# Performance work log

Measured on AMD Instinct MI355X. Metric: run time of the kernel, lower is better.

Reference implementation:

```python
import jax, jax.numpy as jnp
import numpy as np

# Dimensions (all layers are mLSTM due to the constructor bug: `if w` tests the
# whole truthy `which` list, so signature=(2,1) still yields 3 mLSTM layers).
L, S, B, I = 3, 512, 4, 512      # layers, seq_len, batch, inp_dim
H, D = 8, 64                     # head_num, head_dim
HD = H * D                       # hidden dim = 512
P = 2 * I                        # up_l projection dim (m-branch p_factor = 2)
K = 4                            # causal conv kernel size
EPS = 1e-5
PNAMES = ['ln_g', 'ln_b', 'upl_w', 'upl_b', 'upr_w', 'upr_b', 'conv_w', 'conv_b',
          'wq_w', 'wq_b', 'wk_w', 'wk_b', 'wv_w', 'wv_b', 'wo_w', 'wo_b',
          'wi_w', 'wi_b', 'wf_w', 'wf_b', 'skip_w', 'gn_g', 'gn_b', 'down_w', 'down_b']


def setup_inputs() -> dict:
    key = jax.random.key(0)
    ks = iter(jax.random.split(key, 16))
    def w(shape, fan_in):
        return jax.random.normal(next(ks), shape, jnp.float32) / np.float32(np.sqrt(fan_in))
    return {
        'seq': jax.random.normal(next(ks), (S, B, I), jnp.float32),
        'ln_g': jnp.ones((L, I), jnp.float32), 'ln_b': jnp.zeros((L, I), jnp.float32),
        'upl_w': w((L, P, I), I), 'upl_b': jnp.zeros((L, P), jnp.float32),
        'upr_w': w((L, HD, I), I), 'upr_b': jnp.zeros((L, HD), jnp.float32),
        'conv_w': w((L, K), K), 'conv_b': jnp.zeros((L,), jnp.float32),
        'wq_w': w((L, HD, P), P), 'wq_b': jnp.zeros((L, HD), jnp.float32),
        'wk_w': w((L, HD, P), P), 'wk_b': jnp.zeros((L, HD), jnp.float32),
        'wv_w': w((L, HD, P), P), 'wv_b': jnp.zeros((L, HD), jnp.float32),
        'wo_w': w((L, HD, P), P), 'wo_b': jnp.zeros((L, HD), jnp.float32),
        'wi_w': w((L, H, P), P), 'wi_b': jnp.zeros((L, H), jnp.float32),
        'wf_w': w((L, H, P), P), 'wf_b': jnp.zeros((L, H), jnp.float32),
        'skip_w': w((L, HD, P), P),
        'gn_g': jnp.ones((L, HD), jnp.float32), 'gn_b': jnp.zeros((L, HD), jnp.float32),
        'down_w': w((L, I, HD), HD), 'down_b': jnp.zeros((L, I), jnp.float32),
    }


def _layernorm(x, g, b):
    mu = x.mean(-1, keepdims=True)
    v = ((x - mu) ** 2).mean(-1, keepdims=True)
    return (x - mu) / jnp.sqrt(v + EPS) * g + b


def _groupnorm(x, g, b):
    # GroupNorm(head_num, HD) on (B, HD): normalize each head's D channels
    xh = x.reshape(-1, H, D)
    mu = xh.mean(-1, keepdims=True)
    v = ((xh - mu) ** 2).mean(-1, keepdims=True)
    xn = (xh - mu) / jnp.sqrt(v + EPS)
    return (xn * g.reshape(H, D) + b.reshape(H, D)).reshape(-1, HD)


def _causal_conv(x, w, b):
    # 1-channel causal conv over the feature axis of the per-step vector (B, P)
    xp = jnp.pad(x, ((0, 0), (K - 1, 0)))
    y = b
    for k in range(K):  # K=4, static unroll
        y = y + w[k] * xp[:, k:k + x.shape[1]]
    return y


def _mlstm_step(p, x, state):
    c_, n_, m_ = state
    x_n = _layernorm(x, p['ln_g'], p['ln_b'])
    x_t = x_n @ p['upl_w'].T + p['upl_b']                 # (B, P)
    r_t = x_n @ p['upr_w'].T + p['upr_b']                 # (B, HD)
    x_c = jax.nn.silu(_causal_conv(x_t, p['conv_w'], p['conv_b']))
    q = (x_c @ p['wq_w'].T + p['wq_b']).reshape(-1, H, D)
    k = (x_c @ p['wk_w'].T + p['wk_b']).reshape(-1, H, D) / np.float32(np.sqrt(D))
    v = (x_t @ p['wv_w'].T + p['wv_b']).reshape(-1, H, D)
    i = x_c @ p['wi_w'].T + p['wi_b']                     # (B, H)
    f = x_c @ p['wf_w'].T + p['wf_b']                     # (B, H)
    o = jax.nn.sigmoid(x_t @ p['wo_w'].T + p['wo_b'])     # (B, HD)
    m = jnp.maximum(f + m_, i)                            # stabilizer
    ig = jnp.exp(i - m)
    fg = jnp.exp(f - m + m_)
    c = fg[..., None, None] * c_ + ig[..., None, None] * jnp.einsum('bhd,bhe->bhde', v, k)
    n = fg[..., None] * n_ + ig[..., None] * k
    num = jnp.einsum('bhde,bhe->bhd', c, q)
    den = jnp.maximum(jnp.abs(jnp.einsum('bhd,bhd->bh', n, q)), 1.0)[..., None]
    h = o * (num / den).reshape(-1, HD)
    out = _groupnorm(h, p['gn_g'], p['gn_b']) + x_c @ p['skip_w'].T
    out = out * jax.nn.silu(r_t)
    out = out @ p['down_w'].T + p['down_b']
    return out + x, (c, n, m)


def _forward(seq, params):
    b = seq.shape[1]
    def step(states, x_t):
        new_states = []
        inp = x_t
        for l in range(L):
            pl = {k: v[l] for k, v in params.items()}
            inp, st = _mlstm_step(pl, inp, states[l])
            new_states.append(st)
        return tuple(new_states), inp
    init = tuple((jnp.zeros((b, H, D, D), seq.dtype),
                  jnp.ones((b, H, D), seq.dtype),
                  jnp.zeros((b, H), seq.dtype)) for _ in range(L))
    _, out = jax.lax.scan(step, init, seq)
    return out  # (S, B, I)


def reference(seq, ln_g, ln_b, upl_w, upl_b, upr_w, upr_b, conv_w, conv_b,
              wq_w, wq_b, wk_w, wk_b, wv_w, wv_b, wo_w, wo_b,
              wi_w, wi_b, wf_w, wf_b, skip_w, gn_g, gn_b, down_w, down_b):
    params = dict(zip(PNAMES, [ln_g, ln_b, upl_w, upl_b, upr_w, upr_b, conv_w, conv_b,
                               wq_w, wq_b, wk_w, wk_b, wv_w, wv_b, wo_w, wo_b,
                               wi_w, wi_b, wf_w, wf_b, skip_w, gn_g, gn_b, down_w, down_b]))
    return _forward(seq, params)
```

## Files before the change

### kernel.cpp

```cpp
#include <hip/hip_runtime.h>
#include <hip/hip_bf16.h>
#include <cstdint>
#include <cstddef>

typedef short short8 __attribute__((ext_vector_type(8)));
typedef short short4v __attribute__((ext_vector_type(4)));
typedef float f32x4 __attribute__((ext_vector_type(4)));
typedef __hip_bfloat16 bf16;

#define NROW 2048
#define N1 1536
#define N2 1664
#define N3 1024
#define EPSV 1e-5f

static __device__ __forceinline__ bf16 f2bf(float v){ return __float2bfloat16(v); }
static __device__ __forceinline__ float bfbits2f(short s){
  unsigned u = ((unsigned)(unsigned short)s) << 16;
  float f; __builtin_memcpy(&f, &u, 4); return f;
}
static __device__ __forceinline__ void split_bf(float v, bf16& h, bf16& l){
  h = __float2bfloat16(v);
  l = __float2bfloat16(v - __bfloat162float(h));
}

static __device__ __forceinline__ void gload16(const bf16* g, bf16* l){
  __builtin_amdgcn_global_load_lds(
      (const __attribute__((address_space(1))) void*)(g),
      (__attribute__((address_space(3))) void*)(l), 16, 0, 0);
}

#define MFMA __builtin_amdgcn_mfma_f32_16x16x32_bf16

__global__ __launch_bounds__(256) void pack_all(
    const float* __restrict__ upl, const float* __restrict__ upr,
    const float* __restrict__ wq,  const float* __restrict__ wk,
    const float* __restrict__ skp, const float* __restrict__ wi,
    const float* __restrict__ wf,  const float* __restrict__ wv,
    const float* __restrict__ wo,  const float* __restrict__ dw,
    const float* __restrict__ uplb, const float* __restrict__ uprb,
    const float* __restrict__ wqb,  const float* __restrict__ wkb,
    const float* __restrict__ wib,  const float* __restrict__ wfb,
    const float* __restrict__ wvb,  const float* __restrict__ wob,
    const float* __restrict__ dwb,
    bf16* __restrict__ W1h, bf16* __restrict__ W1l,
    bf16* __restrict__ W2h, bf16* __restrict__ W2l,
    bf16* __restrict__ W3h, bf16* __restrict__ W3l,
    bf16* __restrict__ W4h, bf16* __restrict__ W4l,
    float* __restrict__ b1, float* __restrict__ b2,
    float* __restrict__ b3, float* __restrict__ b4)
{
  int l = blockIdx.y;
  int bx = blockIdx.x;
  if (bx < 1536){
    int r = bx;
    const float* src = (r < 1024) ? upl + ((size_t)l*1024 + r)*512
                                  : upr + ((size_t)l*512 + (r-1024))*512;
    size_t o = ((size_t)l*N1 + r)*512;
    for (int c = threadIdx.x; c < 512; c += 256) split_bf(src[c], W1h[o+c], W1l[o+c]);
  } else if (bx < 3200){
    int r = bx - 1536;
    const float* src; float sc = 1.f;
    if (r < 512)        src = wq  + ((size_t)l*512 + r)*1024;
    else if (r < 1024){ src = wk  + ((size_t)l*512 + r-512)*1024; sc = 0.125f; }
    else if (r < 1536)  src = skp + ((size_t)l*512 + r-1024)*1024;
    else if (r < 1544)  src = wi  + ((size_t)l*8   + r-1536)*1024;
    else if (r < 1552)  src = wf  + ((size_t)l*8   + r-1544)*1024;
    else src = nullptr;
    size_t o = ((size_t)l*N2 + r)*1024;
    for (int c = threadIdx.x; c < 1024; c += 256)
      split_bf(src ? src[c]*sc : 0.f, W2h[o+c], W2l[o+c]);
  } else if (bx < 4224){
    int r = bx - 3200;
    const float* src = (r < 512) ? wv + ((size_t)l*512 + r)*1024
                                 : wo + ((size_t)l*512 + (r-512))*1024;
    size_t o = ((size_t)l*N3 + r)*1024;
    for (int c = threadIdx.x; c < 1024; c += 256) split_bf(src[c], W3h[o+c], W3l[o+c]);
  } else if (bx < 4736){
    int r = bx - 4224;
    const float* src = dw + ((size_t)l*512 + r)*512;
    size_t o = ((size_t)l*512 + r)*512;
    for (int c = threadIdx.x; c < 512; c += 256) split_bf(src[c], W4h[o+c], W4l[o+c]);
  } else {
    for (int j = threadIdx.x; j < N1; j += 256)
      b1[l*N1+j] = (j < 1024) ? uplb[l*1024+j] : uprb[l*512+j-1024];
    for (int j = threadIdx.x; j < N2; j += 256){
      float v = 0.f;
      if (j < 512)        v = wqb[l*512+j];
      else if (j < 1024)  v = wkb[l*512+j-512]*0.125f;
      else if (j < 1536)  v = 0.f;
      else if (j < 1544)  v = wib[l*8+j-1536];
      else if (j < 1552)  v = wfb[l*8+j-1544];
      b2[l*N2+j] = v;
    }
    for (int j = threadIdx.x; j < N3; j += 256)
      b3[l*N3+j] = (j < 512) ? wvb[l*512+j] : wob[l*512+j-512];
    for (int j = threadIdx.x; j < 512; j += 256)
      b4[l*512+j] = dwb[l*512+j];
  }
}

static __device__ __forceinline__ void gemm_core(
    bf16* __restrict__ sm,
    int bx, int by,
    const bf16* __restrict__ Ah, const bf16* __restrict__ Al,
    const bf16* __restrict__ Wh, const bf16* __restrict__ Wl,
    const float* __restrict__ bias, float* __restrict__ Cf,
    bf16* __restrict__ Cbh, bf16* __restrict__ Cbl,
    const float* __restrict__ resid, int N, int K)
{
  int tid = threadIdx.x;
  int lane = tid & 63, w = tid >> 6;
  int wr = w >> 2, wc = w & 3;
  int m0 = by*128, n0 = bx*128;
  int srow = tid >> 2, sslot = tid & 3;
  int gcol = ((sslot ^ (srow & 3)) * 8);
  const bf16* gAh = Ah + (size_t)(m0 + srow)*K + gcol;
  const bf16* gAl = Al + (size_t)(m0 + srow)*K + gcol;
  const bf16* gBh = Wh + (size_t)(n0 + srow)*K + gcol;
  const bf16* gBl = Wl + (size_t)(n0 + srow)*K + gcol;

  f32x4 acc[4][2];
  for (int i=0;i<4;i++) for (int j=0;j<2;j++) acc[i][j] = (f32x4){0.f,0.f,0.f,0.f};

  int r = lane & 15, g = lane >> 4;
  int xs = (g ^ (r & 3)) * 8;
  int aoff[4], boff[2];
  for (int mi=0;mi<4;mi++) aoff[mi] = (wr*64 + mi*16 + r)*32 + xs;
  for (int ni=0;ni<2;ni++) boff[ni] = (wc*32 + ni*16 + r)*32 + xs;

  int nt = K >> 5;
#define STAGE_T(base, kk) do{ bf16* _d = sm + (base) + tid*8; \
    gload16(gAh + (kk), _d); \
    gload16(gAl + (kk), _d + 4096); \
    gload16(gBh + (kk), _d + 8192); \
    gload16(gBl + (kk), _d + 12288); }while(0)

  STAGE_T(0, 0);
  asm volatile("s_waitcnt vmcnt(0)" ::: "memory");
  __builtin_amdgcn_s_barrier();

  for (int t = 0; t < nt; ++t){
    int cb = (t & 1) * 16384;
    if (t + 1 < nt) STAGE_T(16384 - cb, (t+1)*32);
    const bf16* sA = sm + cb;
    short8 ah[4], al[4], bh2[2], bl2[2];
    for (int mi=0;mi<4;mi++){
      ah[mi] = *(const short8*)(sA + aoff[mi]);
      al[mi] = *(const short8*)(sA + 4096 + aoff[mi]);
    }
    for (int ni=0;ni<2;ni++){
      bh2[ni] = *(const short8*)(sA + 8192 + boff[ni]);
      bl2[ni] = *(const short8*)(sA + 12288 + boff[ni]);
    }
    for (int mi=0;mi<4;mi++) for (int ni=0;ni<2;ni++)
      acc[mi][ni] = MFMA(ah[mi], bh2[ni], acc[mi][ni],0,0,0);
    for (int mi=0;mi<4;mi++) for (int ni=0;ni<2;ni++)
      acc[mi][ni] = MFMA(al[mi], bh2[ni], acc[mi][ni],0,0,0);
    for (int mi=0;mi<4;mi++) for (int ni=0;ni<2;ni++)
      acc[mi][ni] = MFMA(ah[mi], bl2[ni], acc[mi][ni],0,0,0);
    asm volatile("s_waitcnt vmcnt(0)" ::: "memory");
    __builtin_amdgcn_s_barrier();
  }
#undef STAGE_T

  for (int mi=0;mi<4;mi++) for (int ni=0;ni<2;ni++){
    int col = n0 + wc*32 + ni*16 + r;
    float bv = bias ? bias[col] : 0.f;
    for (int j=0;j<4;j++){
      int row = m0 + wr*64 + mi*16 + g*4 + j;
      float v = acc[mi][ni][j] + bv;
      size_t o = (size_t)row*N + col;
      if (resid) v += resid[o];
      if (Cf) Cf[o] = v;
      if (Cbh) split_bf(v, Cbh[o], Cbl[o]);
    }
  }
}

static __device__ __forceinline__ void gemm_core64(
    bf16* __restrict__ sm,
    int bx, int by,
    const bf16* __restrict__ Ah, const bf16* __restrict__ Al,
    const bf16* __restrict__ Wh, const bf16* __restrict__ Wl,
    const float* __restrict__ bias, float* __restrict__ Cf,
    bf16* __restrict__ Cbh, bf16* __restrict__ Cbl,
    const float* __restrict__ resid, int N, int K)
{
  int tid = threadIdx.x;
  int lane = tid & 63, w = tid >> 6;
  int m0 = by*64, n0 = bx*128;
  int srow = tid >> 2, sslot = tid & 3;
  int gcol = ((sslot ^ (srow & 3)) * 8);
  const bf16* gAh = Ah + (size_t)(m0 + srow)*K + gcol;
  const bf16* gAl = Al + (size_t)(m0 + srow)*K + gcol;
  const bf16* gBh = Wh + (size_t)(n0 + srow)*K + gcol;
  const bf16* gBl = Wl + (size_t)(n0 + srow)*K + gcol;
  size_t pstr = (size_t)64*K;

  f32x4 acc[4][2];
  for (int i=0;i<4;i++) for (int j=0;j<2;j++) acc[i][j] = (f32x4){0.f,0.f,0.f,0.f};

  int r = lane & 15, g = lane >> 4;
  int xs = (g ^ (r & 3)) * 8;
  int aoff[4], boff[2];
  for (int mi=0;mi<4;mi++) aoff[mi] = (mi*16 + r)*32 + xs;
  for (int ni=0;ni<2;ni++) boff[ni] = (w*32 + ni*16 + r)*32 + xs;

  int nt = K >> 5;
#define STAGE64(base, kk) do{ bf16* _d = sm + (base) + tid*8; \
    gload16(gAh + (kk), _d); \
    gload16(gAl + (kk), _d + 2048); \
    gload16(gBh + (kk), _d + 4096);  gload16(gBh + (kk) + pstr, _d + 6144); \
    gload16(gBl + (kk), _d + 8192);  gload16(gBl + (kk) + pstr, _d + 10240); }while(0)

  STAGE64(0, 0);
  asm volatile("s_waitcnt vmcnt(0)" ::: "memory");
  __builtin_amdgcn_s_barrier();

  for (int t = 0; t < nt; ++t){
    int cb = (t & 1) * 12288;
    if (t + 1 < nt) STAGE64(12288 - cb, (t+1)*32);
    const bf16* sA = sm + cb;
    short8 ah[4], al[4], bh2[2], bl2[2];
    for (int mi=0;mi<4;mi++){
      ah[mi] = *(const short8*)(sA + aoff[mi]);
      al[mi] = *(const short8*)(sA + 2048 + aoff[mi]);
    }
    for (int ni=0;ni<2;ni++){
      bh2[ni] = *(const short8*)(sA + 4096 + boff[ni]);
      bl2[ni] = *(const short8*)(sA + 8192 + boff[ni]);
    }
    for (int mi=0;mi<4;mi++) for (int ni=0;ni<2;ni++)
      acc[mi][ni] = MFMA(ah[mi], bh2[ni], acc[mi][ni],0,0,0);
    for (int mi=0;mi<4;mi++) for (int ni=0;ni<2;ni++)
      acc[mi][ni] = MFMA(al[mi], bh2[ni], acc[mi][ni],0,0,0);
    for (int mi=0;mi<4;mi++) for (int ni=0;ni<2;ni++)
      acc[mi][ni] = MFMA(ah[mi], bl2[ni], acc[mi][ni],0,0,0);
    asm volatile("s_waitcnt vmcnt(0)" ::: "memory");
    __builtin_amdgcn_s_barrier();
  }
#undef STAGE64

  for (int mi=0;mi<4;mi++) for (int ni=0;ni<2;ni++){
    int col = n0 + w*32 + ni*16 + r;
    float bv = bias ? bias[col] : 0.f;
    for (int j=0;j<4;j++){
      int row = m0 + mi*16 + g*4 + j;
      float v = acc[mi][ni][j] + bv;
      size_t o = (size_t)row*N + col;
      if (resid) v += resid[o];
      if (Cf) Cf[o] = v;
      if (Cbh) split_bf(v, Cbh[o], Cbl[o]);
    }
  }
}

__global__ __launch_bounds__(512) void gemm_std(
    const bf16* __restrict__ Ah, const bf16* __restrict__ Al,
    const bf16* __restrict__ Wh, const bf16* __restrict__ Wl,
    const float* __restrict__ bias, float* __restrict__ Cf,
    bf16* __restrict__ Cbh, bf16* __restrict__ Cbl,
    const float* __restrict__ resid, int N, int K, int nbx)
{
  __shared__ bf16 sm[2*4*4096];
  int id = blockIdx.x;
  int cpx = gridDim.x >> 3;
  int swz = (id & 7)*cpx + (id >> 3);
  int by = swz / nbx, bx = swz - by*nbx;
  gemm_core(sm, bx, by, Ah, Al, Wh, Wl, bias, Cf, Cbh, Cbl, resid, N, K);
}

__global__ __launch_bounds__(256) void gemm_s64(
    const bf16* __restrict__ Ah, const bf16* __restrict__ Al,
    const bf16* __restrict__ Wh, const bf16* __restrict__ Wl,
    const float* __restrict__ bias, float* __restrict__ Cf,
    bf16* __restrict__ Cbh, bf16* __restrict__ Cbl,
    const float* __restrict__ resid, int N, int K, int nbx)
{
  __shared__ bf16 sm[2*12288];
  int id = blockIdx.x;
  int cpx = gridDim.x >> 3;
  int swz = (id & 7)*cpx + (id >> 3);
  int by = swz / nbx, bx = swz - by*nbx;
  gemm_core64(sm, bx, by, Ah, Al, Wh, Wl, bias, Cf, Cbh, Cbl, resid, N, K);
}

__global__ __launch_bounds__(512) void gemm23(
    const bf16* __restrict__ A2h, const bf16* __restrict__ A2l,
    const bf16* __restrict__ W2h, const bf16* __restrict__ W2l,
    const float* __restrict__ b2,
    bf16* __restrict__ c2h, bf16* __restrict__ c2l,
    const bf16* __restrict__ A3h, const bf16* __restrict__ A3l,
    const bf16* __restrict__ W3h, const bf16* __restrict__ W3l,
    const float* __restrict__ b3,
    bf16* __restrict__ c3h, bf16* __restrict__ c3l)
{
  __shared__ bf16 sm[2*4*4096];
  int id = blockIdx.x;
  int cpx = gridDim.x >> 3;
  int swz = (id & 7)*cpx + (id >> 3);
  int by = swz / 21, bx = swz - by*21;
  if (bx < 13)
    gemm_core(sm, bx, by, A2h, A2l, W2h, W2l, b2, nullptr, c2h, c2l, nullptr, N2, 1024);
  else
    gemm_core(sm, bx-13, by, A3h, A3l, W3h, W3l, b3, nullptr, c3h, c3l, nullptr, N3, 1024);
}

__global__ __launch_bounds__(256) void ln_kernel(const float* __restrict__ x,
    const float* __restrict__ g, const float* __restrict__ bt,
    bf16* __restrict__ xnh, bf16* __restrict__ xnl)
{
  int row = blockIdx.x, t = threadIdx.x;
  float v0 = x[(size_t)row*512 + t], v1 = x[(size_t)row*512 + 256 + t];
  float s = v0 + v1, ss = v0*v0 + v1*v1;
  for (int m=1; m<64; m<<=1){ s += __shfl_xor(s,m); ss += __shfl_xor(ss,m); }
  __shared__ float sh[8];
  int w = t >> 6, lane = t & 63;
  if (lane == 0){ sh[w] = s; sh[4+w] = ss; }
  __syncthreads();
  s = sh[0]+sh[1]+sh[2]+sh[3]; ss = sh[4]+sh[5]+sh[6]+sh[7];
  float mu = s*(1.f/512.f), var = ss*(1.f/512.f) - mu*mu;
  float rs = rsqrtf(var + EPSV);
  float y0 = (v0-mu)*rs*g[t]     + bt[t];
  float y1 = (v1-mu)*rs*g[256+t] + bt[256+t];
  split_bf(y0, xnh[(size_t)row*512 + t],       xnl[(size_t)row*512 + t]);
  split_bf(y1, xnh[(size_t)row*512 + 256 + t], xnl[(size_t)row*512 + 256 + t]);
}

__global__ __launch_bounds__(256) void conv_kernel(
    const bf16* __restrict__ c1h, const bf16* __restrict__ c1l,
    const float* __restrict__ cw, const float* __restrict__ cb,
    bf16* __restrict__ xch, bf16* __restrict__ xcl,
    bf16* __restrict__ xth, bf16* __restrict__ xtl)
{
  int row = blockIdx.x;
  size_t rb = (size_t)row*N1;
  float w0=cw[0], w1=cw[1], w2=cw[2], w3=cw[3], bb=cb[0];
  int j0 = threadIdx.x*4;
  float x[7];
  for (int k=0;k<3;k++){
    int j = j0-3+k;
    x[k] = (j>=0) ? (bfbits2f(*(const short*)(c1h+rb+j)) +
                     bfbits2f(*(const short*)(c1l+rb+j))) : 0.f;
  }
  short4v h4 = *(const short4v*)(c1h+rb+j0);
  short4v l4 = *(const short4v*)(c1l+rb+j0);
  for (int k=0;k<4;k++) x[3+k] = bfbits2f(h4[k]) + bfbits2f(l4[k]);
  for (int i=0;i<4;i++){
    float y = bb + w0*x[i] + w1*x[i+1] + w2*x[i+2] + w3*x[i+3];
    float sg = 1.f/(1.f + __expf(-y));
    size_t o = (size_t)row*1024 + j0 + i;
    split_bf(y*sg, xch[o], xcl[o]);
    split_bf(x[3+i], xth[o], xtl[o]);
  }
}

__global__ __launch_bounds__(512) void prep_kernel(
    const bf16* __restrict__ c3h, const bf16* __restrict__ c3l,
    const bf16* __restrict__ c2h, const bf16* __restrict__ c2l,
    bf16* __restrict__ vTh, bf16* __restrict__ vTl,
    float* __restrict__ rowterm, float* __restrict__ colterm)
{
  int bh = blockIdx.y, b = bh >> 3, h = bh & 7;
  if (blockIdx.x < 8){
    int d0 = blockIdx.x*8;
    int s = threadIdx.x;
    for (int dd=0; dd<8; dd++){
      int d = d0 + dd;
      size_t i = (size_t)(s*4+b)*N3 + h*64 + d;
      size_t o = ((size_t)bh*64 + d)*512 + s;
      vTh[o] = c3h[i];
      vTl[o] = c3l[i];
    }
    return;
  }
  if (threadIdx.x >= 64) return;
  int lane = threadIdx.x;
  double fv[8]; float iv[8];
  for (int j=0;j<8;j++){
    int t = lane*8 + j;
    size_t ro = (size_t)(t*4+b)*N2;
    fv[j] = (double)(bfbits2f(*(const short*)(c2h+ro+1544+h)) +
                     bfbits2f(*(const short*)(c2l+ro+1544+h)));
    iv[j] = bfbits2f(*(const short*)(c2h+ro+1536+h)) +
            bfbits2f(*(const short*)(c2l+ro+1536+h));
  }
  double ps[8]; double s = 0.0;
  for (int j=0;j<8;j++){ s += fv[j]; ps[j] = s; }
  double run = s;
  for (int o=1;o<64;o<<=1){
    double u = __shfl_up(run, o);
    if (lane >= o) run += u;
  }
  double excl = run - s;
  float ct[8];
  for (int j=0;j<8;j++){
    ct[j] = (float)((double)iv[j] - (excl + ps[j]));
    colterm[bh*512 + lane*8 + j] = ct[j];
  }
  float pm[8]; float mm = -3.0e38f;
  for (int j=0;j<8;j++){ mm = fmaxf(mm, ct[j]); pm[j] = mm; }
  float incl = mm;
  for (int o=1;o<64;o<<=1){
    float u = __shfl_up(incl, o);
    if (lane >= o) incl = fmaxf(incl, u);
  }
  float ex = __shfl_up(incl, 1);
  if (lane == 0) ex = -3.0e38f;
  for (int j=0;j<8;j++){
    float inc = fmaxf(ex, pm[j]);
    rowterm[bh*512 + lane*8 + j] = -fmaxf(0.f, inc);
  }
}

__global__ __launch_bounds__(256) void attn_kernel(
    const bf16* __restrict__ c2h, const bf16* __restrict__ c2l,
    const bf16* __restrict__ vTh, const bf16* __restrict__ vTl,
    const float* __restrict__ rowt, const float* __restrict__ colt,
    float* __restrict__ num, float* __restrict__ denp)
{
  __shared__ bf16 Ph[32*64], Pl[32*64];
  int lane = threadIdx.x & 63, w = threadIdx.x >> 6;
  int tb = blockIdx.x, bh = blockIdx.y, b = bh >> 3, h = bh & 7;
  int t0 = tb*32;
  int r = lane & 15, g = lane >> 4;
  int rq = g*4;

  short8 qh[2][2], ql[2][2];
  for (int mi=0;mi<2;mi++) for (int k0=0;k0<2;k0++){
    size_t off = (size_t)((t0+mi*16+r)*4+b)*N2 + h*64 + k0*32 + g*8;
    qh[mi][k0] = *(const short8*)(c2h+off);
    ql[mi][k0] = *(const short8*)(c2l+off);
  }
  const float* rt = rowt + bh*512;
  const float* ctm = colt + bh*512;
  float rtv[2][4];
  for (int mi=0;mi<2;mi++) for (int j=0;j<4;j++) rtv[mi][j] = rt[t0+mi*16+rq+j];

  f32x4 accPV[2];
  for (int i=0;i<2;i++) accPV[i] = (f32x4){0.f,0.f,0.f,0.f};
  float rsum[2][4];
  for (int i=0;i<2;i++) for (int j=0;j<4;j++) rsum[i][j] = 0.f;

  int nsb = (tb >> 1) + 1;
  for (int sb=0; sb<nsb; ++sb){
    int s0 = sb*64;
    f32x4 acc[2];
    for (int i=0;i<2;i++) acc[i] = (f32x4){0.f,0.f,0.f,0.f};
    short8 kh[2], kl[2];
    for (int k0=0;k0<2;k0++){
      size_t off = (size_t)((s0+w*16+r)*4+b)*N2 + 512 + h*64 + k0*32 + g*8;
      kh[k0] = *(const short8*)(c2h+off);
      kl[k0] = *(const short8*)(c2l+off);
    }
    for (int k0=0;k0<2;k0++){
      for (int mi=0;mi<2;mi++) acc[mi] = MFMA(qh[mi][k0], kh[k0], acc[mi],0,0,0);
      for (int mi=0;mi<2;mi++) acc[mi] = MFMA(ql[mi][k0], kh[k0], acc[mi],0,0,0);
      for (int mi=0;mi<2;mi++) acc[mi] = MFMA(qh[mi][k0], kl[k0], acc[mi],0,0,0);
    }
    int sl = w*16 + r;
    int s = s0 + sl;
    float ctv = ctm[s];
    for (int mi=0;mi<2;mi++){
      for (int j=0;j<4;j++){
        int tloc = mi*16 + rq + j;
        int t = t0 + tloc;
        float wg = (s <= t) ? __expf(rtv[mi][j] + ctv) : 0.f;
        float gv = acc[mi][j] * wg;
        rsum[mi][j] += gv;
        int col = ((((sl>>3) ^ (tloc&7))<<3) | (sl&7));
        split_bf(gv, Ph[tloc*64+col], Pl[tloc*64+col]);
      }
    }
    __syncthreads();
    short8 vh[2], vl[2];
    for (int k0=0;k0<2;k0++){
      size_t off = ((size_t)bh*64 + w*16 + r)*512 + s0 + k0*32 + g*8;
      vh[k0] = *(const short8*)(vTh+off);
      vl[k0] = *(const short8*)(vTl+off);
    }
    for (int k0=0;k0<2;k0++){
      short8 ph[2], pl[2];
      for (int mi=0;mi<2;mi++){
        int tloc = mi*16 + r;
        int slot = (k0*4 + g) ^ (tloc&7);
        ph[mi] = *(const short8*)(&Ph[tloc*64 + slot*8]);
        pl[mi] = *(const short8*)(&Pl[tloc*64 + slot*8]);
      }
      for (int mi=0;mi<2;mi++) accPV[mi] = MFMA(ph[mi], vh[k0], accPV[mi],0,0,0);
      for (int mi=0;mi<2;mi++) accPV[mi] = MFMA(pl[mi], vh[k0], accPV[mi],0,0,0);
      for (int mi=0;mi<2;mi++) accPV[mi] = MFMA(ph[mi], vl[k0], accPV[mi],0,0,0);
    }
    __syncthreads();
  }

  for (int mi=0;mi<2;mi++)
    for (int j=0;j<4;j++){
      int t = t0 + mi*16 + rq + j;
      num[((size_t)bh*512 + t)*64 + w*16 + r] = accPV[mi][j];
    }
  for (int mi=0;mi<2;mi++)
    for (int j=0;j<4;j++){
      float v = rsum[mi][j];
      v += __shfl_xor(v,1); v += __shfl_xor(v,2);
      v += __shfl_xor(v,4); v += __shfl_xor(v,8);
      if (r == 0){
        int t = t0 + mi*16 + rq + j;
        denp[((size_t)bh*512 + t)*4 + w] = v;
      }
    }
}

__global__ __launch_bounds__(512) void h_kernel(
    const float* __restrict__ num, const float* __restrict__ denp,
    const float* __restrict__ rowt,
    const bf16* __restrict__ c2h, const bf16* __restrict__ c2l,
    const bf16* __restrict__ c3h, const bf16* __restrict__ c3l,
    const bf16* __restrict__ c1h, const bf16* __restrict__ c1l,
    const float* __restrict__ gng, const float* __restrict__ gnb,
    bf16* __restrict__ oph, bf16* __restrict__ opl)
{
  int row = blockIdx.x, t = row >> 2, b = row & 3;
  int h = threadIdx.x >> 6, d = threadIdx.x & 63;
  int bh = b*8 + h;
  size_t bt = (size_t)bh*512 + t;
  size_t qo = (size_t)row*N2 + h*64 + d;
  float qs = bfbits2f(*(const short*)(c2h+qo)) + bfbits2f(*(const short*)(c2l+qo));
  for (int m=1; m<64; m<<=1) qs += __shfl_xor(qs, m);
  float dn = __expf(rowt[bt]) * qs;
  for (int p=0; p<4; p++) dn += denp[bt*4 + p];
  dn = fmaxf(fabsf(dn), 1.f);
  float nv = num[bt*64 + d];
  size_t io = (size_t)row*N3 + 512 + h*64 + d;
  float ov = bfbits2f(*(const short*)(c3h+io)) + bfbits2f(*(const short*)(c3l+io));
  float o = 1.f/(1.f + __expf(-ov));
  float hv = o * nv / dn;
  float s = hv, ss = hv*hv;
  for (int m=1; m<64; m<<=1){ s += __shfl_xor(s,m); ss += __shfl_xor(ss,m); }
  float mu = s*(1.f/64.f), var = ss*(1.f/64.f) - mu*mu;
  float gn = (hv - mu)*rsqrtf(var + EPSV)*gng[h*64+d] + gnb[h*64+d];
  size_t ks = (size_t)row*N2 + 1024 + h*64 + d;
  float sk = bfbits2f(*(const short*)(c2h+ks)) + bfbits2f(*(const short*)(c2l+ks));
  size_t kr = (size_t)row*N1 + 1024 + h*64 + d;
  float rv = bfbits2f(*(const short*)(c1h+kr)) + bfbits2f(*(const short*)(c1l+kr));
  float y = (gn + sk) * (rv/(1.f + __expf(-rv)));
  size_t oo = (size_t)row*512 + h*64 + d;
  split_bf(y, oph[oo], opl[oo]);
}

extern "C" void kernel_launch(void* const* d_in, const int* in_sizes, int n_in,
                              void* d_out, int out_size, void* d_ws, size_t ws_size,
                              hipStream_t stream)
{
  (void)in_sizes; (void)n_in; (void)out_size; (void)ws_size;
  const float* seq    = (const float*)d_in[0];
  const float* ln_g   = (const float*)d_in[1];
  const float* ln_b   = (const float*)d_in[2];
  const float* upl_w  = (const float*)d_in[3];
  const float* upl_b  = (const float*)d_in[4];
  const float* upr_w  = (const float*)d_in[5];
  const float* upr_b  = (const float*)d_in[6];
  const float* conv_w = (const float*)d_in[7];
  const float* conv_b = (const float*)d_in[8];
  const float* wq_w   = (const float*)d_in[9];
  const float* wq_b   = (const float*)d_in[10];
  const float* wk_w   = (const float*)d_in[11];
  const float* wk_b   = (const float*)d_in[12];
  const float* wv_w   = (const float*)d_in[13];
  const float* wv_b   = (const float*)d_in[14];
  const float* wo_w   = (const float*)d_in[15];
  const float* wo_b   = (const float*)d_in[16];
  const float* wi_w   = (const float*)d_in[17];
  const float* wi_b   = (const float*)d_in[18];
  const float* wf_w   = (const float*)d_in[19];
  const float* wf_b   = (const float*)d_in[20];
  const float* skip_w = (const float*)d_in[21];
  const float* gn_g   = (const float*)d_in[22];
  const float* gn_b   = (const float*)d_in[23];
  const float* down_w = (const float*)d_in[24];
  const float* down_b = (const float*)d_in[25];

  char* ws = (char*)d_ws;
  size_t off = 0;
  auto alloc = [&](size_t bytes)->char*{
    char* p = ws + off; off = (off + bytes + 255) & ~(size_t)255; return p;
  };
  bf16*  W1h = (bf16*)alloc((size_t)3*N1*512*2);
  bf16*  W1l = (bf16*)alloc((size_t)3*N1*512*2);
  bf16*  W2h = (bf16*)alloc((size_t)3*N2*1024*2);
  bf16*  W2l = (bf16*)alloc((size_t)3*N2*1024*2);
  bf16*  W3h = (bf16*)alloc((size_t)3*N3*1024*2);
  bf16*  W3l = (bf16*)alloc((size_t)3*N3*1024*2);
  bf16*  W4h = (bf16*)alloc((size_t)3*512*512*2);
  bf16*  W4l = (bf16*)alloc((size_t)3*512*512*2);
  float* b1  = (float*)alloc((size_t)3*N1*4);
  float* b2  = (float*)alloc((size_t)3*N2*4);
  float* b3  = (float*)alloc((size_t)3*N3*4);
  float* b4  = (float*)alloc((size_t)3*512*4);
  bf16*  xnh = (bf16*)alloc((size_t)NROW*512*2);
  bf16*  xnl = (bf16*)alloc((size_t)NROW*512*2);
  bf16*  c1h = (bf16*)alloc((size_t)NROW*N1*2);
  bf16*  c1l = (bf16*)alloc((size_t)NROW*N1*2);
  bf16*  xth = (bf16*)alloc((size_t)NROW*1024*2);
  bf16*  xtl = (bf16*)alloc((size_t)NROW*1024*2);
  bf16*  xch = (bf16*)alloc((size_t)NROW*1024*2);
  bf16*  xcl = (bf16*)alloc((size_t)NROW*1024*2);
  bf16*  c2h = (bf16*)alloc((size_t)NROW*N2*2);
  bf16*  c2l = (bf16*)alloc((size_t)NROW*N2*2);
  bf16*  c3h = (bf16*)alloc((size_t)NROW*N3*2);
  bf16*  c3l = (bf16*)alloc((size_t)NROW*N3*2);
  bf16*  vTh = (bf16*)alloc((size_t)32*64*512*2);
  bf16*  vTl = (bf16*)alloc((size_t)32*64*512*2);
  float* rowt= (float*)alloc((size_t)32*512*4);
  float* colt= (float*)alloc((size_t)32*512*4);
  float* denp= (float*)alloc((size_t)32*512*4*4);
  float* num = (float*)alloc((size_t)32*512*64*4);
  bf16*  oph = (bf16*)alloc((size_t)NROW*512*2);
  bf16*  opl = (bf16*)alloc((size_t)NROW*512*2);
  float* xA  = (float*)alloc((size_t)NROW*512*4);
  float* xB  = (float*)alloc((size_t)NROW*512*4);

  pack_all<<<dim3(4737,3), 256, 0, stream>>>(
      upl_w, upr_w, wq_w, wk_w, skip_w, wi_w, wf_w, wv_w, wo_w, down_w,
      upl_b, upr_b, wq_b, wk_b, wi_b, wf_b, wv_b, wo_b, down_b,
      W1h, W1l, W2h, W2l, W3h, W3l, W4h, W4l, b1, b2, b3, b4);

  for (int l = 0; l < 3; l++){
    const float* x_in = (l == 0) ? seq : ((l == 1) ? xA : xB);
    float* x_out = (l == 0) ? xA : ((l == 1) ? xB : (float*)d_out);

    ln_kernel<<<NROW, 256, 0, stream>>>(x_in, ln_g + l*512, ln_b + l*512, xnh, xnl);
    gemm_s64<<<32*12, 256, 0, stream>>>(
        xnh, xnl, W1h + (size_t)l*N1*512, W1l + (size_t)l*N1*512,
        b1 + l*N1, nullptr, c1h, c1l, nullptr, N1, 512, 12);
    conv_kernel<<<NROW, 256, 0, stream>>>(c1h, c1l, conv_w + l*4, conv_b + l,
                                          xch, xcl, xth, xtl);
    gemm23<<<21*16, 512, 0, stream>>>(
        xch, xcl, W2h + (size_t)l*N2*1024, W2l + (size_t)l*N2*1024, b2 + l*N2,
        c2h, c2l,
        xth, xtl, W3h + (size_t)l*N3*1024, W3l + (size_t)l*N3*1024, b3 + l*N3,
        c3h, c3l);
    prep_kernel<<<dim3(9,32), 512, 0, stream>>>(c3h, c3l, c2h, c2l,
                                                vTh, vTl, rowt, colt);
    attn_kernel<<<dim3(16,32), 256, 0, stream>>>(c2h, c2l, vTh, vTl,
                                                 rowt, colt, num, denp);
    h_kernel<<<NROW, 512, 0, stream>>>(num, denp, rowt, c2h, c2l, c3h, c3l,
                                       c1h, c1l, gn_g + l*512, gn_b + l*512,
                                       oph, opl);
    gemm_s64<<<32*4, 256, 0, stream>>>(
        oph, opl, W4h + (size_t)l*512*512, W4l + (size_t)l*512*512,
        b4 + l*512, x_out, nullptr, nullptr, x_in, 512, 512, 4);
  }
}
```

Measured before the change: 410.0 us.

## Fuse prep kernel into GEMM epilogue and attention, drop xt copy

Removes prep_kernel. The V transpose moves into the gemm23 epilogue as scattered stores, and the gate cumsum/max prefix scan is recomputed per attention block into shared memory. The conv kernel no longer writes a separate xt copy; gemm23 reads the c1 buffer directly with a leading-dimension stride. Weight packing is also vectorised with 4-wide loads and stores. The changes save one launch and several intermediate global round-trips, at the cost of uncoalesced transposed stores in the epilogue and redundant scan work in every attention block.

```diff
diff --git a/kernel.cpp b/kernel.cpp
--- a/kernel.cpp
+++ b/kernel.cpp
@@ -52,12 +52,18 @@
 {
   int l = blockIdx.y;
   int bx = blockIdx.x;
+  int c4 = threadIdx.x;
   if (bx < 1536){
+    if (c4 >= 128) return;
     int r = bx;
     const float* src = (r < 1024) ? upl + ((size_t)l*1024 + r)*512
                                   : upr + ((size_t)l*512 + (r-1024))*512;
-    size_t o = ((size_t)l*N1 + r)*512;
-    for (int c = threadIdx.x; c < 512; c += 256) split_bf(src[c], W1h[o+c], W1l[o+c]);
+    size_t o = ((size_t)l*N1 + r)*512 + c4*4;
+    f32x4 v = *(const f32x4*)(src + c4*4);
+    short4v hh, ll;
+    for (int e=0;e<4;e++){ bf16 h_,l_; split_bf(v[e],h_,l_);
+      hh[e] = *(short*)&h_; ll[e] = *(short*)&l_; }
+    *(short4v*)(W1h+o) = hh; *(short4v*)(W1l+o) = ll;
   } else if (bx < 3200){
     int r = bx - 1536;
     const float* src; float sc = 1.f;
@@ -67,20 +73,32 @@
     else if (r < 1544)  src = wi  + ((size_t)l*8   + r-1536)*1024;
     else if (r < 1552)  src = wf  + ((size_t)l*8   + r-1544)*1024;
     else src = nullptr;
-    size_t o = ((size_t)l*N2 + r)*1024;
-    for (int c = threadIdx.x; c < 1024; c += 256)
-      split_bf(src ? src[c]*sc : 0.f, W2h[o+c], W2l[o+c]);
+    size_t o = ((size_t)l*N2 + r)*1024 + c4*4;
+    f32x4 v = src ? *(const f32x4*)(src + c4*4) : (f32x4){0.f,0.f,0.f,0.f};
+    short4v hh, ll;
+    for (int e=0;e<4;e++){ bf16 h_,l_; split_bf(v[e]*sc,h_,l_);
+      hh[e] = *(short*)&h_; ll[e] = *(short*)&l_; }
+    *(short4v*)(W2h+o) = hh; *(short4v*)(W2l+o) = ll;
   } else if (bx < 4224){
     int r = bx - 3200;
     const float* src = (r < 512) ? wv + ((size_t)l*512 + r)*1024
                                  : wo + ((size_t)l*512 + (r-512))*1024;
-    size_t o = ((size_t)l*N3 + r)*1024;
-    for (int c = threadIdx.x; c < 1024; c += 256) split_bf(src[c], W3h[o+c], W3l[o+c]);
+    size_t o = ((size_t)l*N3 + r)*1024 + c4*4;
+    f32x4 v = *(const f32x4*)(src + c4*4);
+    short4v hh, ll;
+    for (int e=0;e<4;e++){ bf16 h_,l_; split_bf(v[e],h_,l_);
+      hh[e] = *(short*)&h_; ll[e] = *(short*)&l_; }
+    *(short4v*)(W3h+o) = hh; *(short4v*)(W3l+o) = ll;
   } else if (bx < 4736){
+    if (c4 >= 128) return;
     int r = bx - 4224;
     const float* src = dw + ((size_t)l*512 + r)*512;
-    size_t o = ((size_t)l*512 + r)*512;
-    for (int c = threadIdx.x; c < 512; c += 256) split_bf(src[c], W4h[o+c], W4l[o+c]);
+    size_t o = ((size_t)l*512 + r)*512 + c4*4;
+    f32x4 v = *(const f32x4*)(src + c4*4);
+    short4v hh, ll;
+    for (int e=0;e<4;e++){ bf16 h_,l_; split_bf(v[e],h_,l_);
+      hh[e] = *(short*)&h_; ll[e] = *(short*)&l_; }
+    *(short4v*)(W4h+o) = hh; *(short4v*)(W4l+o) = ll;
   } else {
     for (int j = threadIdx.x; j < N1; j += 256)
       b1[l*N1+j] = (j < 1024) ? uplb[l*1024+j] : uprb[l*512+j-1024];
@@ -107,7 +125,8 @@
     const bf16* __restrict__ Wh, const bf16* __restrict__ Wl,
     const float* __restrict__ bias, float* __restrict__ Cf,
     bf16* __restrict__ Cbh, bf16* __restrict__ Cbl,
-    const float* __restrict__ resid, int N, int K)
+    const float* __restrict__ resid, int N, int K, int lda,
+    bf16* __restrict__ vTh, bf16* __restrict__ vTl)
 {
   int tid = threadIdx.x;
   int lane = tid & 63, w = tid >> 6;
@@ -115,8 +134,8 @@
   int m0 = by*128, n0 = bx*128;
   int srow = tid >> 2, sslot = tid & 3;
   int gcol = ((sslot ^ (srow & 3)) * 8);
-  const bf16* gAh = Ah + (size_t)(m0 + srow)*K + gcol;
-  const bf16* gAl = Al + (size_t)(m0 + srow)*K + gcol;
+  const bf16* gAh = Ah + (size_t)(m0 + srow)*lda + gcol;
+  const bf16* gAl = Al + (size_t)(m0 + srow)*lda + gcol;
   const bf16* gBh = Wh + (size_t)(n0 + srow)*K + gcol;
   const bf16* gBl = Wl + (size_t)(n0 + srow)*K + gcol;
 
@@ -173,7 +192,17 @@
       size_t o = (size_t)row*N + col;
       if (resid) v += resid[o];
       if (Cf) Cf[o] = v;
-      if (Cbh) split_bf(v, Cbh[o], Cbl[o]);
+      if (Cbh){
+        bf16 h_, l_;
+        split_bf(v, h_, l_);
+        Cbh[o] = h_; Cbl[o] = l_;
+        if (vTh){
+          int hh = col >> 6, dd = col & 63;
+          int tt = row >> 2, bb = row & 3;
+          size_t vo = ((size_t)(bb*8+hh)*64 + dd)*512 + tt;
+          vTh[vo] = h_; vTl[vo] = l_;
+        }
+      }
     }
   }
 }
@@ -185,15 +214,15 @@
     const bf16* __restrict__ Wh, const bf16* __restrict__ Wl,
     const float* __restrict__ bias, float* __restrict__ Cf,
     bf16* __restrict__ Cbh, bf16* __restrict__ Cbl,
-    const float* __restrict__ resid, int N, int K)
+    const float* __restrict__ resid, int N, int K, int lda)
 {
   int tid = threadIdx.x;
   int lane = tid & 63, w = tid >> 6;
   int m0 = by*64, n0 = bx*128;
   int srow = tid >> 2, sslot = tid & 3;
   int gcol = ((sslot ^ (srow & 3)) * 8);
-  const bf16* gAh = Ah + (size_t)(m0 + srow)*K + gcol;
-  const bf16* gAl = Al + (size_t)(m0 + srow)*K + gcol;
+  const bf16* gAh = Ah + (size_t)(m0 + srow)*lda + gcol;
+  const bf16* gAl = Al + (size_t)(m0 + srow)*lda + gcol;
   const bf16* gBh = Wh + (size_t)(n0 + srow)*K + gcol;
   const bf16* gBl = Wl + (size_t)(n0 + srow)*K + gcol;
   size_t pstr = (size_t)64*K;
@@ -256,34 +285,19 @@
   }
 }
 
-__global__ __launch_bounds__(512) void gemm_std(
-    const bf16* __restrict__ Ah, const bf16* __restrict__ Al,
-    const bf16* __restrict__ Wh, const bf16* __restrict__ Wl,
-    const float* __restrict__ bias, float* __restrict__ Cf,
-    bf16* __restrict__ Cbh, bf16* __restrict__ Cbl,
-    const float* __restrict__ resid, int N, int K, int nbx)
-{
-  __shared__ bf16 sm[2*4*4096];
-  int id = blockIdx.x;
-  int cpx = gridDim.x >> 3;
-  int swz = (id & 7)*cpx + (id >> 3);
-  int by = swz / nbx, bx = swz - by*nbx;
-  gemm_core(sm, bx, by, Ah, Al, Wh, Wl, bias, Cf, Cbh, Cbl, resid, N, K);
-}
-
 __global__ __launch_bounds__(256) void gemm_s64(
     const bf16* __restrict__ Ah, const bf16* __restrict__ Al,
     const bf16* __restrict__ Wh, const bf16* __restrict__ Wl,
     const float* __restrict__ bias, float* __restrict__ Cf,
     bf16* __restrict__ Cbh, bf16* __restrict__ Cbl,
-    const float* __restrict__ resid, int N, int K, int nbx)
+    const float* __restrict__ resid, int N, int K, int lda, int nbx)
 {
   __shared__ bf16 sm[2*12288];
   int id = blockIdx.x;
   int cpx = gridDim.x >> 3;
   int swz = (id & 7)*cpx + (id >> 3);
   int by = swz / nbx, bx = swz - by*nbx;
-  gemm_core64(sm, bx, by, Ah, Al, Wh, Wl, bias, Cf, Cbh, Cbl, resid, N, K);
+  gemm_core64(sm, bx, by, Ah, Al, Wh, Wl, bias, Cf, Cbh, Cbl, resid, N, K, lda);
 }
 
 __global__ __launch_bounds__(512) void gemm23(
@@ -294,7 +308,8 @@
     const bf16* __restrict__ A3h, const bf16* __restrict__ A3l,
     const bf16* __restrict__ W3h, const bf16* __restrict__ W3l,
     const float* __restrict__ b3,
-    bf16* __restrict__ c3h, bf16* __restrict__ c3l)
+    bf16* __restrict__ c3h, bf16* __restrict__ c3l,
+    bf16* __restrict__ vTh, bf16* __restrict__ vTl)
 {
   __shared__ bf16 sm[2*4*4096];
   int id = blockIdx.x;
@@ -302,9 +317,14 @@
   int swz = (id & 7)*cpx + (id >> 3);
   int by = swz / 21, bx = swz - by*21;
   if (bx < 13)
-    gemm_core(sm, bx, by, A2h, A2l, W2h, W2l, b2, nullptr, c2h, c2l, nullptr, N2, 1024);
-  else
-    gemm_core(sm, bx-13, by, A3h, A3l, W3h, W3l, b3, nullptr, c3h, c3l, nullptr, N3, 1024);
+    gemm_core(sm, bx, by, A2h, A2l, W2h, W2l, b2, nullptr, c2h, c2l,
+              nullptr, N2, 1024, 1024, nullptr, nullptr);
+  else {
+    int bx3 = bx - 13;
+    gemm_core(sm, bx3, by, A3h, A3l, W3h, W3l, b3, nullptr, c3h, c3l,
+              nullptr, N3, 1024, N1,
+              (bx3 < 4) ? vTh : nullptr, (bx3 < 4) ? vTl : nullptr);
+  }
 }
 
 __global__ __launch_bounds__(256) void ln_kernel(const float* __restrict__ x,
@@ -331,8 +351,7 @@
 __global__ __launch_bounds__(256) void conv_kernel(
     const bf16* __restrict__ c1h, const bf16* __restrict__ c1l,
     const float* __restrict__ cw, const float* __restrict__ cb,
-    bf16* __restrict__ xch, bf16* __restrict__ xcl,
-    bf16* __restrict__ xth, bf16* __restrict__ xtl)
+    bf16* __restrict__ xch, bf16* __restrict__ xcl)
 {
   int row = blockIdx.x;
   size_t rb = (size_t)row*N1;
@@ -352,78 +371,67 @@
     float sg = 1.f/(1.f + __expf(-y));
     size_t o = (size_t)row*1024 + j0 + i;
     split_bf(y*sg, xch[o], xcl[o]);
-    split_bf(x[3+i], xth[o], xtl[o]);
-  }
-}
-
-__global__ __launch_bounds__(512) void prep_kernel(
-    const bf16* __restrict__ c3h, const bf16* __restrict__ c3l,
-    const bf16* __restrict__ c2h, const bf16* __restrict__ c2l,
-    bf16* __restrict__ vTh, bf16* __restrict__ vTl,
-    float* __restrict__ rowterm, float* __restrict__ colterm)
-{
-  int bh = blockIdx.y, b = bh >> 3, h = bh & 7;
-  if (blockIdx.x < 8){
-    int d0 = blockIdx.x*8;
-    int s = threadIdx.x;
-    for (int dd=0; dd<8; dd++){
-      int d = d0 + dd;
-      size_t i = (size_t)(s*4+b)*N3 + h*64 + d;
-      size_t o = ((size_t)bh*64 + d)*512 + s;
-      vTh[o] = c3h[i];
-      vTl[o] = c3l[i];
-    }
-    return;
-  }
-  if (threadIdx.x >= 64) return;
-  int lane = threadIdx.x;
-  double fv[8]; float iv[8];
-  for (int j=0;j<8;j++){
-    int t = lane*8 + j;
-    size_t ro = (size_t)(t*4+b)*N2;
-    fv[j] = (double)(bfbits2f(*(const short*)(c2h+ro+1544+h)) +
-                     bfbits2f(*(const short*)(c2l+ro+1544+h)));
-    iv[j] = bfbits2f(*(const short*)(c2h+ro+1536+h)) +
-            bfbits2f(*(const short*)(c2l+ro+1536+h));
-  }
-  double ps[8]; double s = 0.0;
-  for (int j=0;j<8;j++){ s += fv[j]; ps[j] = s; }
-  double run = s;
-  for (int o=1;o<64;o<<=1){
-    double u = __shfl_up(run, o);
-    if (lane >= o) run += u;
-  }
-  double excl = run - s;
-  float ct[8];
-  for (int j=0;j<8;j++){
-    ct[j] = (float)((double)iv[j] - (excl + ps[j]));
-    colterm[bh*512 + lane*8 + j] = ct[j];
-  }
-  float pm[8]; float mm = -3.0e38f;
-  for (int j=0;j<8;j++){ mm = fmaxf(mm, ct[j]); pm[j] = mm; }
-  float incl = mm;
-  for (int o=1;o<64;o<<=1){
-    float u = __shfl_up(incl, o);
-    if (lane >= o) incl = fmaxf(incl, u);
-  }
-  float ex = __shfl_up(incl, 1);
-  if (lane == 0) ex = -3.0e38f;
-  for (int j=0;j<8;j++){
-    float inc = fmaxf(ex, pm[j]);
-    rowterm[bh*512 + lane*8 + j] = -fmaxf(0.f, inc);
   }
 }
 
 __global__ __launch_bounds__(256) void attn_kernel(
     const bf16* __restrict__ c2h, const bf16* __restrict__ c2l,
     const bf16* __restrict__ vTh, const bf16* __restrict__ vTl,
-    const float* __restrict__ rowt, const float* __restrict__ colt,
+    float* __restrict__ rowt,
     float* __restrict__ num, float* __restrict__ denp)
 {
   __shared__ bf16 Ph[32*64], Pl[32*64];
+  __shared__ float cts[512];
+  __shared__ float rtl[32];
   int lane = threadIdx.x & 63, w = threadIdx.x >> 6;
-  int tb = blockIdx.x, bh = blockIdx.y, b = bh >> 3, h = bh & 7;
+  int x = blockIdx.x;
+  int tb = (x & 1) ? (15 - (x >> 1)) : (x >> 1);
+  int bh = blockIdx.y, b = bh >> 3, h = bh & 7;
   int t0 = tb*32;
+
+  if (w == 0){
+    double fv[8]; float iv[8];
+    for (int j=0;j<8;j++){
+      int t = lane*8 + j;
+      size_t ro = (size_t)(t*4+b)*N2;
+      fv[j] = (double)(bfbits2f(*(const short*)(c2h+ro+1544+h)) +
+                       bfbits2f(*(const short*)(c2l+ro+1544+h)));
+      iv[j] = bfbits2f(*(const short*)(c2h+ro+1536+h)) +
+              bfbits2f(*(const short*)(c2l+ro+1536+h));
+    }
+    double ps[8]; double s = 0.0;
+    for (int j=0;j<8;j++){ s += fv[j]; ps[j] = s; }
+    double run = s;
+    for (int o=1;o<64;o<<=1){
+      double u = __shfl_up(run, o);
+      if (lane >= o) run += u;
+    }
+    double excl = run - s;
+    float ct[8];
+    for (int j=0;j<8;j++){
+      ct[j] = (float)((double)iv[j] - (excl + ps[j]));
+      cts[lane*8+j] = ct[j];
+    }
+    float pm[8]; float mm = -3.0e38f;
+    for (int j=0;j<8;j++){ mm = fmaxf(mm, ct[j]); pm[j] = mm; }
+    float incl = mm;
+    for (int o=1;o<64;o<<=1){
+      float u = __shfl_up(incl, o);
+      if (lane >= o) incl = fmaxf(incl, u);
+    }
+    float ex = __shfl_up(incl, 1);
+    if (lane == 0) ex = -3.0e38f;
+    for (int j=0;j<8;j++){
+      int t = lane*8 + j;
+      float rt_ = -fmaxf(0.f, fmaxf(ex, pm[j]));
+      if (t >= t0 && t < t0+32){
+        rtl[t - t0] = rt_;
+        rowt[bh*512 + t] = rt_;
+      }
+    }
+  }
+  __syncthreads();
+
   int r = lane & 15, g = lane >> 4;
   int rq = g*4;
 
@@ -433,10 +441,8 @@
     qh[mi][k0] = *(const short8*)(c2h+off);
     ql[mi][k0] = *(const short8*)(c2l+off);
   }
-  const float* rt = rowt + bh*512;
-  const float* ctm = colt + bh*512;
   float rtv[2][4];
-  for (int mi=0;mi<2;mi++) for (int j=0;j<4;j++) rtv[mi][j] = rt[t0+mi*16+rq+j];
+  for (int mi=0;mi<2;mi++) for (int j=0;j<4;j++) rtv[mi][j] = rtl[mi*16+rq+j];
 
   f32x4 accPV[2];
   for (int i=0;i<2;i++) accPV[i] = (f32x4){0.f,0.f,0.f,0.f};
@@ -461,7 +467,7 @@
     }
     int sl = w*16 + r;
     int s = s0 + sl;
-    float ctv = ctm[s];
+    float ctv = cts[s];
     for (int mi=0;mi<2;mi++){
       for (int j=0;j<4;j++){
         int tloc = mi*16 + rq + j;
@@ -602,8 +608,6 @@
   bf16*  xnl = (bf16*)alloc((size_t)NROW*512*2);
   bf16*  c1h = (bf16*)alloc((size_t)NROW*N1*2);
   bf16*  c1l = (bf16*)alloc((size_t)NROW*N1*2);
-  bf16*  xth = (bf16*)alloc((size_t)NROW*1024*2);
-  bf16*  xtl = (bf16*)alloc((size_t)NROW*1024*2);
   bf16*  xch = (bf16*)alloc((size_t)NROW*1024*2);
   bf16*  xcl = (bf16*)alloc((size_t)NROW*1024*2);
   bf16*  c2h = (bf16*)alloc((size_t)NROW*N2*2);
@@ -613,7 +617,6 @@
   bf16*  vTh = (bf16*)alloc((size_t)32*64*512*2);
   bf16*  vTl = (bf16*)alloc((size_t)32*64*512*2);
   float* rowt= (float*)alloc((size_t)32*512*4);
-  float* colt= (float*)alloc((size_t)32*512*4);
   float* denp= (float*)alloc((size_t)32*512*4*4);
   float* num = (float*)alloc((size_t)32*512*64*4);
   bf16*  oph = (bf16*)alloc((size_t)NROW*512*2);
@@ -633,23 +636,21 @@
     ln_kernel<<<NROW, 256, 0, stream>>>(x_in, ln_g + l*512, ln_b + l*512, xnh, xnl);
     gemm_s64<<<32*12, 256, 0, stream>>>(
         xnh, xnl, W1h + (size_t)l*N1*512, W1l + (size_t)l*N1*512,
-        b1 + l*N1, nullptr, c1h, c1l, nullptr, N1, 512, 12);
+        b1 + l*N1, nullptr, c1h, c1l, nullptr, N1, 512, 512, 12);
     conv_kernel<<<NROW, 256, 0, stream>>>(c1h, c1l, conv_w + l*4, conv_b + l,
-                                          xch, xcl, xth, xtl);
+                                          xch, xcl);
     gemm23<<<21*16, 512, 0, stream>>>(
         xch, xcl, W2h + (size_t)l*N2*1024, W2l + (size_t)l*N2*1024, b2 + l*N2,
         c2h, c2l,
-        xth, xtl, W3h + (size_t)l*N3*1024, W3l + (size_t)l*N3*1024, b3 + l*N3,
-        c3h, c3l);
-    prep_kernel<<<dim3(9,32), 512, 0, stream>>>(c3h, c3l, c2h, c2l,
-                                                vTh, vTl, rowt, colt);
+        c1h, c1l, W3h + (size_t)l*N3*1024, W3l + (size_t)l*N3*1024, b3 + l*N3,
+        c3h, c3l, vTh, vTl);
     attn_kernel<<<dim3(16,32), 256, 0, stream>>>(c2h, c2l, vTh, vTl,
-                                                 rowt, colt, num, denp);
+                                                 rowt, num, denp);
     h_kernel<<<NROW, 512, 0, stream>>>(num, denp, rowt, c2h, c2l, c3h, c3l,
                                        c1h, c1l, gn_g + l*512, gn_b + l*512,
                                        oph, opl);
     gemm_s64<<<32*4, 256, 0, stream>>>(
         oph, opl, W4h + (size_t)l*512*512, W4l + (size_t)l*512*512,
-        b4 + l*512, x_out, nullptr, nullptr, x_in, 512, 512, 4);
-  }
-}
+        b4 + l*512, x_out, nullptr, nullptr, x_in, 512, 512, 512, 4);
+  }
+}
```

Result: slower. 427.0 us (+4.2%).
